# Kernel optimization log

Measured on AMD Instinct MI355X. Metric: run time of the kernel, lower is better.

Reference implementation:

```python
import jax, jax.numpy as jnp
import numpy as np

B = 1024   # batch
N = 8192   # code length (power of 2)
K = 4096   # info bits


def polar_transform(v):
    """Recursive XOR butterfly (polar encoding), vectorized.

    Faithful to the TF loop: at each stage every length-L block is split into
    positions 0::2 ('odd') and 1::2 ('even'); output block = [odd^even, even].
    v: (B, N, 1) int32 in {0,1}. Returns (B, N, 1).
    """
    b, n, _ = v.shape
    blocks, L = 1, n
    while L > 1:
        vv = v.reshape(b, blocks, L // 2, 2, 1)
        odd = vv[:, :, :, 0, :]   # in-block indices 0,2,4,...
        even = vv[:, :, :, 1, :]  # in-block indices 1,3,5,...
        xor = (odd + even) % 2    # tf.math.floormod(V_odd + V_even, 2)
        v = jnp.concatenate([xor, even], axis=2).reshape(b, blocks * L, 1)
        blocks *= 2
        L //= 2
    return v


def setup_inputs() -> dict:
    key = jax.random.key(0)
    k1, k2 = jax.random.split(key)
    # info bits as float 0/1 (kept float so the bwd variant has a float primal)
    info_bits = jnp.round(jax.random.uniform(k1, (B, K), dtype=jnp.float32))
    # hoisted tf.random.uniform(..., maxval=2, dtype=int32)
    u_random = jax.random.randint(k2, (B, N), 0, 2, dtype=jnp.int32)
    # info_set = sorted top-K entries of the reliability permutation
    perm = np.random.RandomState(0).permutation(N)
    info_set = jnp.asarray(np.sort(perm[:K]).astype(np.int32))
    return {"info_bits": info_bits, "u_random": u_random, "info_set": info_set}


def reference(info_bits, u_random, info_set):
    # scatter info bits into the random word at the info positions
    u2d = u_random.at[:, info_set].set(info_bits.astype(jnp.int32))
    # frozen-indicator word: info positions marked with 2
    f2d = u_random.at[:, info_set].set(2)
    u = u2d[..., None]          # (B, N, 1)
    f = f2d[..., None]          # (B, N, 1)
    x = polar_transform(u)      # (B, N, 1)
    r = jnp.stack((1 - u_random, u_random), axis=-1).astype(jnp.float32)  # (B,N,2)
    p = jnp.full((B, N, 2), 0.5, dtype=jnp.float32)
    return x, f, u, p, r
```

## Files before the change

kernel.cpp:

```cpp
#include <hip/hip_runtime.h>
#include <hip/hip_bf16.h>
#include <stdint.h>

#define BB 1024
#define NN 8192
#define KK 4096

typedef float vf4 __attribute__((ext_vector_type(4)));
typedef int   vi4 __attribute__((ext_vector_type(4)));
typedef int   vi2 __attribute__((ext_vector_type(2)));

__global__ void init_pos_kernel(int* __restrict__ pos) {
    int i = blockIdx.x * blockDim.x + threadIdx.x;
    if (i < NN) pos[i] = -1;
}
__global__ void scatter_pos_kernel(const int* __restrict__ info_set, int* __restrict__ pos) {
    int k = blockIdx.x * blockDim.x + threadIdx.x;
    if (k < KK) pos[info_set[k]] = k;
}

__device__ __forceinline__ vf4 mk4(float a, float b, float c, float d) {
    vf4 v; v.x = a; v.y = b; v.z = c; v.w = d; return v;
}

__global__ __launch_bounds__(512) void polar_main_kernel(
    const float* __restrict__ info_bits,
    const int*   __restrict__ u_random,
    const int*   __restrict__ pos,
    float*       __restrict__ out)
{
    __shared__ uint32_t yw[256];

    const int b    = blockIdx.x;
    const int t    = threadIdx.x;
    const int lane = t & 63;
    const int ww   = t >> 6;

    vf4* x4 = (vf4*)(out)                 + (size_t)b * (NN / 4);
    vf4* f4 = (vf4*)(out + (size_t)BB*NN) + (size_t)b * (NN / 4);
    vf4* u4 = (vf4*)(out + 2ull*BB*NN)    + (size_t)b * (NN / 4);
    vf4* p4 = (vf4*)(out + 3ull*BB*NN)    + (size_t)b * (NN / 2);
    vf4* r4 = (vf4*)(out + 5ull*BB*NN)    + (size_t)b * (NN / 2);

    const vi4*   ur4p  = (const vi4*)(u_random + (size_t)b * NN);
    const vi2*   ur2p  = (const vi2*)(u_random + (size_t)b * NN);
    const vi4*   pos4p = (const vi4*)pos;
    const float* ibrow = info_bits + (size_t)b * KK;

    #pragma unroll
    for (int it = 0; it < 4; ++it) {
        const int idx4 = it * 512 + t;
        const vi4 ur = ur4p[idx4];
        const vi4 kk = pos4p[idx4];

        int u0 = ur.x, u1 = ur.y, u2 = ur.z, u3 = ur.w;
        int f0 = u0,   f1 = u1,   f2 = u2,   f3 = u3;
        if (kk.x >= 0) { u0 = ibrow[kk.x] > 0.5f; f0 = 2; }
        if (kk.y >= 0) { u1 = ibrow[kk.y] > 0.5f; f1 = 2; }
        if (kk.z >= 0) { u2 = ibrow[kk.z] > 0.5f; f2 = 2; }
        if (kk.w >= 0) { u3 = ibrow[kk.w] > 0.5f; f3 = 2; }

        u4[idx4] = mk4((float)u0, (float)u1, (float)u2, (float)u3);
        f4[idx4] = mk4((float)f0, (float)f1, (float)f2, (float)f3);

        uint32_t x = (uint32_t)(u0 | (u1 << 1) | (u2 << 2) | (u3 << 3));
        x |= ((uint32_t)__shfl_xor((int)x, 1)) << 4;
        x |= ((uint32_t)__shfl_xor((int)x, 2)) << 8;
        x |= ((uint32_t)__shfl_xor((int)x, 4)) << 16;
        if ((lane & 7) == 0)
            yw[it * 64 + ww * 8 + (lane >> 3)] = x;
    }
    __syncthreads();

    if (ww == 0) {
        uint32_t W0 = yw[lane];
        uint32_t W1 = yw[lane + 64];
        uint32_t W2 = yw[lane + 128];
        uint32_t W3 = yw[lane + 192];

        #define INWORD(W) \
            W ^= (W >> 1)  & 0x55555555u; \
            W ^= (W >> 2)  & 0x33333333u; \
            W ^= (W >> 4)  & 0x0F0F0F0Fu; \
            W ^= (W >> 8)  & 0x00FF00FFu; \
            W ^= (W >> 16) & 0x0000FFFFu;
        INWORD(W0) INWORD(W1) INWORD(W2) INWORD(W3)
        #undef INWORD

        #pragma unroll
        for (int wb = 0; wb < 6; ++wb) {
            const bool keep = ((lane >> wb) & 1);
            uint32_t p0 = (uint32_t)__shfl_xor((int)W0, 1 << wb);
            uint32_t p1 = (uint32_t)__shfl_xor((int)W1, 1 << wb);
            uint32_t p2 = (uint32_t)__shfl_xor((int)W2, 1 << wb);
            uint32_t p3 = (uint32_t)__shfl_xor((int)W3, 1 << wb);
            if (!keep) { W0 ^= p0; W1 ^= p1; W2 ^= p2; W3 ^= p3; }
        }

        W0 ^= W1; W2 ^= W3;
        W0 ^= W2; W1 ^= W3;

        yw[lane]       = W0;
        yw[lane + 64]  = W1;
        yw[lane + 128] = W2;
        yw[lane + 192] = W3;
    }
    __syncthreads();

    #pragma unroll
    for (int it = 0; it < 4; ++it) {
        const int s = it * 512 + t;
        const uint32_t q = __builtin_bitreverse32((uint32_t)s) >> 21;
        const int w   = (int)(q >> 5);
        const int bsh = (int)(q & 31u);
        const float x0 = (float)((yw[w]       >> bsh) & 1u);
        const float x1 = (float)((yw[w + 128] >> bsh) & 1u);
        const float x2 = (float)((yw[w + 64]  >> bsh) & 1u);
        const float x3 = (float)((yw[w + 192] >> bsh) & 1u);
        x4[s] = mk4(x0, x1, x2, x3);
    }

    #pragma unroll
    for (int c = 0; c < 8; ++c) {
        const int j = c * 512 + t;
        const vi2 ur = ur2p[j];
        r4[j] = mk4((float)(1 - ur.x), (float)ur.x,
                    (float)(1 - ur.y), (float)ur.y);
    }

    const vf4 half = mk4(0.5f, 0.5f, 0.5f, 0.5f);
    #pragma unroll
    for (int c = 0; c < 8; ++c)
        p4[c * 512 + t] = half;
}

extern "C" void kernel_launch(void* const* d_in, const int* in_sizes, int n_in,
                              void* d_out, int out_size, void* d_ws, size_t ws_size,
                              hipStream_t stream) {
    const float* info_bits = (const float*)d_in[0];
    const int*   u_random  = (const int*)  d_in[1];
    const int*   info_set  = (const int*)  d_in[2];
    float*       out       = (float*)d_out;
    int*         pos       = (int*)d_ws;

    init_pos_kernel<<<NN / 256, 256, 0, stream>>>(pos);
    scatter_pos_kernel<<<KK / 256, 256, 0, stream>>>(info_set, pos);
    polar_main_kernel<<<BB, 512, 0, stream>>>(info_bits, u_random, pos, out);
}
```

Measured before the change: 272.1 us.

## Split into bit-pack/butterfly kernel and separate float expansion kernel

Splits the single fused kernel into two. A 64-thread-per-row kernel packs u and u_random into bitwords, runs the polar butterfly, and writes packed words to workspace. A 512-thread kernel then expands those bits into all float outputs, using a precomputed frozen bitmask. The aim is to separate the latency-bound packing and butterfly stage from the bandwidth-bound output writes, and to stop idle waves sitting in the butterfly phase. In exchange it adds extra launches and a workspace round trip, and the pack kernel has low occupancy.

```diff
diff --git a/kernel.cpp b/kernel.cpp
--- a/kernel.cpp
+++ b/kernel.cpp
@@ -10,6 +10,13 @@
 typedef int   vi4 __attribute__((ext_vector_type(4)));
 typedef int   vi2 __attribute__((ext_vector_type(2)));
 
+#define POS_OFF    0
+#define FROZEN_OFF (32*1024)
+#define U_OFF      (64*1024)
+#define R_OFF      (64*1024 + 1024*1024)
+#define Y_OFF      (64*1024 + 2*1024*1024)
+#define WS_NEED    (64*1024 + 3*1024*1024)
+
 __global__ void init_pos_kernel(int* __restrict__ pos) {
     int i = blockIdx.x * blockDim.x + threadIdx.x;
     if (i < NN) pos[i] = -1;
@@ -18,9 +25,165 @@
     int k = blockIdx.x * blockDim.x + threadIdx.x;
     if (k < KK) pos[info_set[k]] = k;
 }
+__global__ void frozen_kernel(const int* __restrict__ pos, uint32_t* __restrict__ frozen) {
+    const int gi   = blockIdx.x * blockDim.x + threadIdx.x;
+    const int lane = threadIdx.x & 63;
+    unsigned long long m = __ballot(pos[gi] >= 0);
+    if (lane == 0) {
+        const int w = gi >> 5;
+        frozen[w]     = (uint32_t)m;
+        frozen[w + 1] = (uint32_t)(m >> 32);
+    }
+}
 
 __device__ __forceinline__ vf4 mk4(float a, float b, float c, float d) {
     vf4 v; v.x = a; v.y = b; v.z = c; v.w = d; return v;
+}
+__device__ __forceinline__ uint32_t merge8(uint32_t x) {
+    x |= ((uint32_t)__shfl_xor((int)x, 1)) << 4;
+    x |= ((uint32_t)__shfl_xor((int)x, 2)) << 8;
+    x |= ((uint32_t)__shfl_xor((int)x, 4)) << 16;
+    return x;
+}
+
+__global__ __launch_bounds__(64) void pack_butterfly_kernel(
+    const float* __restrict__ info_bits,
+    const int*   __restrict__ u_random,
+    const int*   __restrict__ pos,
+    uint32_t*    __restrict__ wsu,
+    uint32_t*    __restrict__ wsr,
+    uint32_t*    __restrict__ wsy)
+{
+    __shared__ uint32_t ywu[256];
+    __shared__ uint32_t ywr[256];
+
+    const int b    = blockIdx.x;
+    const int lane = threadIdx.x;
+
+    const vi4*   ur4p  = (const vi4*)(u_random + (size_t)b * NN);
+    const vi4*   pos4p = (const vi4*)pos;
+    const float* ibrow = info_bits + (size_t)b * KK;
+
+    #pragma unroll 8
+    for (int it = 0; it < 32; ++it) {
+        const int idx4 = it * 64 + lane;
+        const vi4 ur = ur4p[idx4];
+        const vi4 kk = pos4p[idx4];
+
+        int u0 = ur.x, u1 = ur.y, u2 = ur.z, u3 = ur.w;
+        if (kk.x >= 0) u0 = ibrow[kk.x] > 0.5f;
+        if (kk.y >= 0) u1 = ibrow[kk.y] > 0.5f;
+        if (kk.z >= 0) u2 = ibrow[kk.z] > 0.5f;
+        if (kk.w >= 0) u3 = ibrow[kk.w] > 0.5f;
+
+        uint32_t xu = merge8((uint32_t)(u0 | (u1 << 1) | (u2 << 2) | (u3 << 3)));
+        uint32_t xr = merge8((uint32_t)(ur.x | (ur.y << 1) | (ur.z << 2) | (ur.w << 3)));
+        if ((lane & 7) == 0) {
+            ywu[it * 8 + (lane >> 3)] = xu;
+            ywr[it * 8 + (lane >> 3)] = xr;
+        }
+    }
+    __syncthreads();
+
+    uint32_t W0 = ywu[lane];
+    uint32_t W1 = ywu[lane + 64];
+    uint32_t W2 = ywu[lane + 128];
+    uint32_t W3 = ywu[lane + 192];
+
+    uint32_t* su = wsu + (size_t)b * 256;
+    uint32_t* sr = wsr + (size_t)b * 256;
+    su[lane] = W0; su[lane + 64] = W1; su[lane + 128] = W2; su[lane + 192] = W3;
+    sr[lane]       = ywr[lane];
+    sr[lane + 64]  = ywr[lane + 64];
+    sr[lane + 128] = ywr[lane + 128];
+    sr[lane + 192] = ywr[lane + 192];
+
+    #define INWORD(W) \
+        W ^= (W >> 1)  & 0x55555555u; \
+        W ^= (W >> 2)  & 0x33333333u; \
+        W ^= (W >> 4)  & 0x0F0F0F0Fu; \
+        W ^= (W >> 8)  & 0x00FF00FFu; \
+        W ^= (W >> 16) & 0x0000FFFFu;
+    INWORD(W0) INWORD(W1) INWORD(W2) INWORD(W3)
+    #undef INWORD
+
+    #pragma unroll
+    for (int wb = 0; wb < 6; ++wb) {
+        const bool keep = ((lane >> wb) & 1);
+        uint32_t p0 = (uint32_t)__shfl_xor((int)W0, 1 << wb);
+        uint32_t p1 = (uint32_t)__shfl_xor((int)W1, 1 << wb);
+        uint32_t p2 = (uint32_t)__shfl_xor((int)W2, 1 << wb);
+        uint32_t p3 = (uint32_t)__shfl_xor((int)W3, 1 << wb);
+        if (!keep) { W0 ^= p0; W1 ^= p1; W2 ^= p2; W3 ^= p3; }
+    }
+    W0 ^= W1; W2 ^= W3;
+    W0 ^= W2; W1 ^= W3;
+
+    uint32_t* sy = wsy + (size_t)b * 256;
+    sy[lane] = W0; sy[lane + 64] = W1; sy[lane + 128] = W2; sy[lane + 192] = W3;
+}
+
+__global__ __launch_bounds__(512) void expand_kernel(
+    const uint32_t* __restrict__ wsu,
+    const uint32_t* __restrict__ wsr,
+    const uint32_t* __restrict__ wsy,
+    const uint32_t* __restrict__ frozen,
+    float*          __restrict__ out)
+{
+    const int b = blockIdx.x;
+    const int t = threadIdx.x;
+
+    vf4* x4 = (vf4*)(out)                 + (size_t)b * (NN / 4);
+    vf4* f4 = (vf4*)(out + (size_t)BB*NN) + (size_t)b * (NN / 4);
+    vf4* u4 = (vf4*)(out + 2ull*BB*NN)    + (size_t)b * (NN / 4);
+    vf4* p4 = (vf4*)(out + 3ull*BB*NN)    + (size_t)b * (NN / 2);
+    vf4* r4 = (vf4*)(out + 5ull*BB*NN)    + (size_t)b * (NN / 2);
+
+    const uint32_t* yu = wsu + (size_t)b * 256;
+    const uint32_t* yr = wsr + (size_t)b * 256;
+    const uint32_t* yy = wsy + (size_t)b * 256;
+
+    #pragma unroll
+    for (int it = 0; it < 4; ++it) {
+        const int idx4 = it * 512 + t;
+        const int w  = idx4 >> 3;
+        const int sh = (idx4 & 7) * 4;
+        const uint32_t wu = yu[w] >> sh;
+        const uint32_t wf = frozen[w] >> sh;
+        const float u0 = (float)(wu & 1u),        u1 = (float)((wu >> 1) & 1u);
+        const float u2 = (float)((wu >> 2) & 1u), u3 = (float)((wu >> 3) & 1u);
+        u4[idx4] = mk4(u0, u1, u2, u3);
+        f4[idx4] = mk4((wf & 1u)        ? 2.0f : u0,
+                       ((wf >> 1) & 1u) ? 2.0f : u1,
+                       ((wf >> 2) & 1u) ? 2.0f : u2,
+                       ((wf >> 3) & 1u) ? 2.0f : u3);
+    }
+
+    #pragma unroll
+    for (int it = 0; it < 4; ++it) {
+        const int s = it * 512 + t;
+        const uint32_t q = __builtin_bitreverse32((uint32_t)s) >> 21;
+        const int w   = (int)(q >> 5);
+        const int bsh = (int)(q & 31u);
+        const float x0 = (float)((yy[w]       >> bsh) & 1u);
+        const float x1 = (float)((yy[w + 128] >> bsh) & 1u);
+        const float x2 = (float)((yy[w + 64]  >> bsh) & 1u);
+        const float x3 = (float)((yy[w + 192] >> bsh) & 1u);
+        x4[s] = mk4(x0, x1, x2, x3);
+    }
+
+    #pragma unroll
+    for (int c = 0; c < 8; ++c) {
+        const int j = c * 512 + t;
+        const uint32_t wr = yr[j >> 4] >> ((j & 15) * 2);
+        const float b0 = (float)(wr & 1u), b1 = (float)((wr >> 1) & 1u);
+        r4[j] = mk4(1.0f - b0, b0, 1.0f - b1, b1);
+    }
+
+    const vf4 half = mk4(0.5f, 0.5f, 0.5f, 0.5f);
+    #pragma unroll
+    for (int c = 0; c < 8; ++c)
+        p4[c * 512 + t] = half;
 }
 
 __global__ __launch_bounds__(512) void polar_main_kernel(
@@ -30,11 +193,8 @@
     float*       __restrict__ out)
 {
     __shared__ uint32_t yw[256];
-
-    const int b    = blockIdx.x;
-    const int t    = threadIdx.x;
-    const int lane = t & 63;
-    const int ww   = t >> 6;
+    const int b = blockIdx.x, t = threadIdx.x;
+    const int lane = t & 63, ww = t >> 6;
 
     vf4* x4 = (vf4*)(out)                 + (size_t)b * (NN / 4);
     vf4* f4 = (vf4*)(out + (size_t)BB*NN) + (size_t)b * (NN / 4);
@@ -42,9 +202,9 @@
     vf4* p4 = (vf4*)(out + 3ull*BB*NN)    + (size_t)b * (NN / 2);
     vf4* r4 = (vf4*)(out + 5ull*BB*NN)    + (size_t)b * (NN / 2);
 
-    const vi4*   ur4p  = (const vi4*)(u_random + (size_t)b * NN);
-    const vi2*   ur2p  = (const vi2*)(u_random + (size_t)b * NN);
-    const vi4*   pos4p = (const vi4*)pos;
+    const vi4* ur4p = (const vi4*)(u_random + (size_t)b * NN);
+    const vi2* ur2p = (const vi2*)(u_random + (size_t)b * NN);
+    const vi4* pos4p = (const vi4*)pos;
     const float* ibrow = info_bits + (size_t)b * KK;
 
     #pragma unroll
@@ -52,32 +212,20 @@
         const int idx4 = it * 512 + t;
         const vi4 ur = ur4p[idx4];
         const vi4 kk = pos4p[idx4];
-
         int u0 = ur.x, u1 = ur.y, u2 = ur.z, u3 = ur.w;
-        int f0 = u0,   f1 = u1,   f2 = u2,   f3 = u3;
+        int f0 = u0, f1 = u1, f2 = u2, f3 = u3;
         if (kk.x >= 0) { u0 = ibrow[kk.x] > 0.5f; f0 = 2; }
         if (kk.y >= 0) { u1 = ibrow[kk.y] > 0.5f; f1 = 2; }
         if (kk.z >= 0) { u2 = ibrow[kk.z] > 0.5f; f2 = 2; }
         if (kk.w >= 0) { u3 = ibrow[kk.w] > 0.5f; f3 = 2; }
-
         u4[idx4] = mk4((float)u0, (float)u1, (float)u2, (float)u3);
         f4[idx4] = mk4((float)f0, (float)f1, (float)f2, (float)f3);
-
-        uint32_t x = (uint32_t)(u0 | (u1 << 1) | (u2 << 2) | (u3 << 3));
-        x |= ((uint32_t)__shfl_xor((int)x, 1)) << 4;
-        x |= ((uint32_t)__shfl_xor((int)x, 2)) << 8;
-        x |= ((uint32_t)__shfl_xor((int)x, 4)) << 16;
-        if ((lane & 7) == 0)
-            yw[it * 64 + ww * 8 + (lane >> 3)] = x;
+        uint32_t x = merge8((uint32_t)(u0 | (u1 << 1) | (u2 << 2) | (u3 << 3)));
+        if ((lane & 7) == 0) yw[it * 64 + ww * 8 + (lane >> 3)] = x;
     }
     __syncthreads();
-
     if (ww == 0) {
-        uint32_t W0 = yw[lane];
-        uint32_t W1 = yw[lane + 64];
-        uint32_t W2 = yw[lane + 128];
-        uint32_t W3 = yw[lane + 192];
-
+        uint32_t W0 = yw[lane], W1 = yw[lane + 64], W2 = yw[lane + 128], W3 = yw[lane + 192];
         #define INWORD(W) \
             W ^= (W >> 1)  & 0x55555555u; \
             W ^= (W >> 2)  & 0x33333333u; \
@@ -86,7 +234,6 @@
             W ^= (W >> 16) & 0x0000FFFFu;
         INWORD(W0) INWORD(W1) INWORD(W2) INWORD(W3)
         #undef INWORD
-
         #pragma unroll
         for (int wb = 0; wb < 6; ++wb) {
             const bool keep = ((lane >> wb) & 1);
@@ -96,38 +243,24 @@
             uint32_t p3 = (uint32_t)__shfl_xor((int)W3, 1 << wb);
             if (!keep) { W0 ^= p0; W1 ^= p1; W2 ^= p2; W3 ^= p3; }
         }
-
-        W0 ^= W1; W2 ^= W3;
-        W0 ^= W2; W1 ^= W3;
-
-        yw[lane]       = W0;
-        yw[lane + 64]  = W1;
-        yw[lane + 128] = W2;
-        yw[lane + 192] = W3;
+        W0 ^= W1; W2 ^= W3; W0 ^= W2; W1 ^= W3;
+        yw[lane] = W0; yw[lane + 64] = W1; yw[lane + 128] = W2; yw[lane + 192] = W3;
     }
     __syncthreads();
-
     #pragma unroll
     for (int it = 0; it < 4; ++it) {
         const int s = it * 512 + t;
         const uint32_t q = __builtin_bitreverse32((uint32_t)s) >> 21;
-        const int w   = (int)(q >> 5);
-        const int bsh = (int)(q & 31u);
-        const float x0 = (float)((yw[w]       >> bsh) & 1u);
-        const float x1 = (float)((yw[w + 128] >> bsh) & 1u);
-        const float x2 = (float)((yw[w + 64]  >> bsh) & 1u);
-        const float x3 = (float)((yw[w + 192] >> bsh) & 1u);
-        x4[s] = mk4(x0, x1, x2, x3);
-    }
-
+        const int w = (int)(q >> 5), bsh = (int)(q & 31u);
+        x4[s] = mk4((float)((yw[w] >> bsh) & 1u), (float)((yw[w + 128] >> bsh) & 1u),
+                    (float)((yw[w + 64] >> bsh) & 1u), (float)((yw[w + 192] >> bsh) & 1u));
+    }
     #pragma unroll
     for (int c = 0; c < 8; ++c) {
         const int j = c * 512 + t;
         const vi2 ur = ur2p[j];
-        r4[j] = mk4((float)(1 - ur.x), (float)ur.x,
-                    (float)(1 - ur.y), (float)ur.y);
-    }
-
+        r4[j] = mk4((float)(1 - ur.x), (float)ur.x, (float)(1 - ur.y), (float)ur.y);
+    }
     const vf4 half = mk4(0.5f, 0.5f, 0.5f, 0.5f);
     #pragma unroll
     for (int c = 0; c < 8; ++c)
@@ -141,9 +274,21 @@
     const int*   u_random  = (const int*)  d_in[1];
     const int*   info_set  = (const int*)  d_in[2];
     float*       out       = (float*)d_out;
-    int*         pos       = (int*)d_ws;
+
+    int*      pos    = (int*)((char*)d_ws + POS_OFF);
+    uint32_t* frozen = (uint32_t*)((char*)d_ws + FROZEN_OFF);
+    uint32_t* wsu    = (uint32_t*)((char*)d_ws + U_OFF);
+    uint32_t* wsr    = (uint32_t*)((char*)d_ws + R_OFF);
+    uint32_t* wsy    = (uint32_t*)((char*)d_ws + Y_OFF);
 
     init_pos_kernel<<<NN / 256, 256, 0, stream>>>(pos);
     scatter_pos_kernel<<<KK / 256, 256, 0, stream>>>(info_set, pos);
-    polar_main_kernel<<<BB, 512, 0, stream>>>(info_bits, u_random, pos, out);
-}
+
+    if (ws_size >= (size_t)WS_NEED) {
+        frozen_kernel<<<NN / 256, 256, 0, stream>>>(pos, frozen);
+        pack_butterfly_kernel<<<BB, 64, 0, stream>>>(info_bits, u_random, pos, wsu, wsr, wsy);
+        expand_kernel<<<BB, 512, 0, stream>>>(wsu, wsr, wsy, frozen, out);
+    } else {
+        polar_main_kernel<<<BB, 512, 0, stream>>>(info_bits, u_random, pos, out);
+    }
+}
```

After: 315.2 us. 15.8% more time.

## Bit-pack u_random in LDS to avoid re-reading it and drop second barrier

Applied to the files above, without the earlier changes.

Packs the u_random bits into a shared bitmask during the first pass, so the r output is built from LDS instead of re-reading u_random from global memory. Every wave now computes the transform redundantly, and the bit-reversed word redistribution uses in-wave shuffles instead of an LDS write and a second __syncthreads. This removes one global read of u_random and a barrier, at the cost of extra shuffles and ALU work in every wave.

```diff
diff --git a/kernel.cpp b/kernel.cpp
--- a/kernel.cpp
+++ b/kernel.cpp
@@ -8,7 +8,6 @@
 
 typedef float vf4 __attribute__((ext_vector_type(4)));
 typedef int   vi4 __attribute__((ext_vector_type(4)));
-typedef int   vi2 __attribute__((ext_vector_type(2)));
 
 __global__ void init_pos_kernel(int* __restrict__ pos) {
     int i = blockIdx.x * blockDim.x + threadIdx.x;
@@ -22,6 +21,12 @@
 __device__ __forceinline__ vf4 mk4(float a, float b, float c, float d) {
     vf4 v; v.x = a; v.y = b; v.z = c; v.w = d; return v;
 }
+__device__ __forceinline__ uint32_t merge8(uint32_t x) {
+    x |= ((uint32_t)__shfl_xor((int)x, 1)) << 4;
+    x |= ((uint32_t)__shfl_xor((int)x, 2)) << 8;
+    x |= ((uint32_t)__shfl_xor((int)x, 4)) << 16;
+    return x;
+}
 
 __global__ __launch_bounds__(512) void polar_main_kernel(
     const float* __restrict__ info_bits,
@@ -29,7 +34,8 @@
     const int*   __restrict__ pos,
     float*       __restrict__ out)
 {
-    __shared__ uint32_t yw[256];
+    __shared__ uint32_t ywu[256];
+    __shared__ uint32_t ywr[256];
 
     const int b    = blockIdx.x;
     const int t    = threadIdx.x;
@@ -43,7 +49,6 @@
     vf4* r4 = (vf4*)(out + 5ull*BB*NN)    + (size_t)b * (NN / 2);
 
     const vi4*   ur4p  = (const vi4*)(u_random + (size_t)b * NN);
-    const vi2*   ur2p  = (const vi2*)(u_random + (size_t)b * NN);
     const vi4*   pos4p = (const vi4*)pos;
     const float* ibrow = info_bits + (size_t)b * KK;
 
@@ -63,69 +68,65 @@
         u4[idx4] = mk4((float)u0, (float)u1, (float)u2, (float)u3);
         f4[idx4] = mk4((float)f0, (float)f1, (float)f2, (float)f3);
 
-        uint32_t x = (uint32_t)(u0 | (u1 << 1) | (u2 << 2) | (u3 << 3));
-        x |= ((uint32_t)__shfl_xor((int)x, 1)) << 4;
-        x |= ((uint32_t)__shfl_xor((int)x, 2)) << 8;
-        x |= ((uint32_t)__shfl_xor((int)x, 4)) << 16;
-        if ((lane & 7) == 0)
-            yw[it * 64 + ww * 8 + (lane >> 3)] = x;
+        uint32_t xu = merge8((uint32_t)(u0 | (u1 << 1) | (u2 << 2) | (u3 << 3)));
+        uint32_t xr = merge8((uint32_t)(ur.x | (ur.y << 1) | (ur.z << 2) | (ur.w << 3)));
+        if ((lane & 7) == 0) {
+            ywu[it * 64 + ww * 8 + (lane >> 3)] = xu;
+            ywr[it * 64 + ww * 8 + (lane >> 3)] = xr;
+        }
     }
     __syncthreads();
 
-    if (ww == 0) {
-        uint32_t W0 = yw[lane];
-        uint32_t W1 = yw[lane + 64];
-        uint32_t W2 = yw[lane + 128];
-        uint32_t W3 = yw[lane + 192];
+    uint32_t W0 = ywu[lane];
+    uint32_t W1 = ywu[lane + 64];
+    uint32_t W2 = ywu[lane + 128];
+    uint32_t W3 = ywu[lane + 192];
 
-        #define INWORD(W) \
-            W ^= (W >> 1)  & 0x55555555u; \
-            W ^= (W >> 2)  & 0x33333333u; \
-            W ^= (W >> 4)  & 0x0F0F0F0Fu; \
-            W ^= (W >> 8)  & 0x00FF00FFu; \
-            W ^= (W >> 16) & 0x0000FFFFu;
-        INWORD(W0) INWORD(W1) INWORD(W2) INWORD(W3)
-        #undef INWORD
+    #define INWORD(W) \
+        W ^= (W >> 1)  & 0x55555555u; \
+        W ^= (W >> 2)  & 0x33333333u; \
+        W ^= (W >> 4)  & 0x0F0F0F0Fu; \
+        W ^= (W >> 8)  & 0x00FF00FFu; \
+        W ^= (W >> 16) & 0x0000FFFFu;
+    INWORD(W0) INWORD(W1) INWORD(W2) INWORD(W3)
+    #undef INWORD
 
-        #pragma unroll
-        for (int wb = 0; wb < 6; ++wb) {
-            const bool keep = ((lane >> wb) & 1);
-            uint32_t p0 = (uint32_t)__shfl_xor((int)W0, 1 << wb);
-            uint32_t p1 = (uint32_t)__shfl_xor((int)W1, 1 << wb);
-            uint32_t p2 = (uint32_t)__shfl_xor((int)W2, 1 << wb);
-            uint32_t p3 = (uint32_t)__shfl_xor((int)W3, 1 << wb);
-            if (!keep) { W0 ^= p0; W1 ^= p1; W2 ^= p2; W3 ^= p3; }
-        }
+    #pragma unroll
+    for (int wb = 0; wb < 6; ++wb) {
+        const bool keep = ((lane >> wb) & 1);
+        uint32_t q0 = (uint32_t)__shfl_xor((int)W0, 1 << wb);
+        uint32_t q1 = (uint32_t)__shfl_xor((int)W1, 1 << wb);
+        uint32_t q2 = (uint32_t)__shfl_xor((int)W2, 1 << wb);
+        uint32_t q3 = (uint32_t)__shfl_xor((int)W3, 1 << wb);
+        if (!keep) { W0 ^= q0; W1 ^= q1; W2 ^= q2; W3 ^= q3; }
+    }
+    W0 ^= W1; W2 ^= W3;
+    W0 ^= W2; W1 ^= W3;
 
-        W0 ^= W1; W2 ^= W3;
-        W0 ^= W2; W1 ^= W3;
-
-        yw[lane]       = W0;
-        yw[lane + 64]  = W1;
-        yw[lane + 128] = W2;
-        yw[lane + 192] = W3;
-    }
-    __syncthreads();
+    const int w = (int)(__builtin_bitreverse32((uint32_t)lane) >> 26);
+    const uint32_t V0 = (uint32_t)__shfl((int)W0, w);
+    const uint32_t V1 = (uint32_t)__shfl((int)W1, w);
+    const uint32_t V2 = (uint32_t)__shfl((int)W2, w);
+    const uint32_t V3 = (uint32_t)__shfl((int)W3, w);
 
     #pragma unroll
     for (int it = 0; it < 4; ++it) {
         const int s = it * 512 + t;
         const uint32_t q = __builtin_bitreverse32((uint32_t)s) >> 21;
-        const int w   = (int)(q >> 5);
         const int bsh = (int)(q & 31u);
-        const float x0 = (float)((yw[w]       >> bsh) & 1u);
-        const float x1 = (float)((yw[w + 128] >> bsh) & 1u);
-        const float x2 = (float)((yw[w + 64]  >> bsh) & 1u);
-        const float x3 = (float)((yw[w + 192] >> bsh) & 1u);
+        const float x0 = (float)((V0 >> bsh) & 1u);
+        const float x1 = (float)((V2 >> bsh) & 1u);
+        const float x2 = (float)((V1 >> bsh) & 1u);
+        const float x3 = (float)((V3 >> bsh) & 1u);
         x4[s] = mk4(x0, x1, x2, x3);
     }
 
     #pragma unroll
     for (int c = 0; c < 8; ++c) {
         const int j = c * 512 + t;
-        const vi2 ur = ur2p[j];
-        r4[j] = mk4((float)(1 - ur.x), (float)ur.x,
-                    (float)(1 - ur.y), (float)ur.y);
+        const uint32_t wr = ywr[j >> 4] >> ((j & 15) * 2);
+        const float b0 = (float)(wr & 1u), b1 = (float)((wr >> 1) & 1u);
+        r4[j] = mk4(1.0f - b0, b0, 1.0f - b1, b1);
     }
 
     const vf4 half = mk4(0.5f, 0.5f, 0.5f, 0.5f);
```

New measurement: 276.3 us. No clear change (+1.5%).
